# Performance work log

Hardware: AMD Instinct MI355X
Metric: run time of the kernel (lower is better)

## Reference

```python
import jax, jax.numpy as jnp
import numpy as np
from jax import lax

EPS = 1e-3  # BatchNorm1d eps from norm_fn
SPARSE_SHAPE = (41, 200, 176)  # (z, y, x)
IN_CH = 4


def _conv3d(x, w, stride, pad):
    # x: [N,C,D,H,W], w: [O,I,kd,kh,kw]
    return lax.conv_general_dilated(x, w, window_strides=stride, padding=pad,
                                    dimension_numbers=('NCDHW', 'OIDHW', 'NCDHW'))


def _bn_relu(y, bn, mask):
    # eval-mode BatchNorm1d over active voxels == per-channel affine; inactive sites
    # must stay exactly 0 in a sparse tensor, hence the final mask multiply.
    g, b, m, v = bn[0], bn[1], bn[2], bn[3]
    scale = g * lax.rsqrt(v + EPS)
    shift = b - m * scale
    y = y * scale[None, :, None, None, None] + shift[None, :, None, None, None]
    return jax.nn.relu(y) * mask


def _subm(x, mask, w, bn):
    # SubMConv3d: conv evaluated only at existing active sites; active set unchanged.
    kd, kh, kw = w.shape[2:]
    pad = [(kd // 2, kd // 2), (kh // 2, kh // 2), (kw // 2, kw // 2)]
    return _bn_relu(_conv3d(x, w, (1, 1, 1), pad), bn, mask)


def _spconv(x, mask, w, bn, stride, pad):
    # SparseConv3d: output active set = sites with >=1 active input in receptive field.
    pads = [(p, p) for p in pad]
    y = _conv3d(x, w, stride, pads)
    k = tuple(w.shape[2:])
    new_mask = lax.reduce_window(mask, 0.0, lax.max, (1, 1) + k, (1, 1) + tuple(stride),
                                 [(0, 0), (0, 0)] + pads)
    new_mask = (new_mask > 0).astype(x.dtype)
    return _bn_relu(y, bn, new_mask), new_mask


def setup_inputs() -> dict:
    key = jax.random.key(0)
    ks = jax.random.split(key, 16)
    D, H, W = SPARSE_SHAPE
    mask = (jax.random.uniform(ks[0], (1, 1, D, H, W)) < 0.02).astype(jnp.float32)
    x = jax.random.normal(ks[1], (1, IN_CH, D, H, W), jnp.float32) * mask
    specs = [(16, IN_CH, (3, 3, 3)), (16, 16, (3, 3, 3)),
             (32, 16, (3, 3, 3)), (32, 32, (3, 3, 3)), (32, 32, (3, 3, 3)),
             (64, 32, (3, 3, 3)), (64, 64, (3, 3, 3)), (64, 64, (3, 3, 3)),
             (64, 64, (3, 3, 3)), (64, 64, (3, 3, 3)), (64, 64, (3, 3, 3)),
             (128, 64, (3, 1, 1))]
    inp = {'x': x, 'mask': mask}
    for i, (co, ci, k) in enumerate(specs):
        kk = jax.random.fold_in(ks[2], i)
        fan = ci * k[0] * k[1] * k[2]
        inp['w%d' % i] = jax.random.normal(kk, (co, ci) + k, jnp.float32) / np.sqrt(fan).astype(np.float32)
        inp['bn%d' % i] = jnp.stack([
            jax.random.uniform(jax.random.fold_in(kk, 1), (co,), minval=0.5, maxval=1.5),
            jax.random.normal(jax.random.fold_in(kk, 2), (co,)) * 0.1,
            jax.random.normal(jax.random.fold_in(kk, 3), (co,)) * 0.1,
            jax.random.uniform(jax.random.fold_in(kk, 4), (co,), minval=0.5, maxval=1.5)])
    return inp


def reference(x, mask, w0, bn0, w1, bn1, w2, bn2, w3, bn3, w4, bn4, w5, bn5,
              w6, bn6, w7, bn7, w8, bn8, w9, bn9, w10, bn10, w11, bn11):
    h = _subm(x, mask, w0, bn0)                       # conv_input (subm1)
    h = _subm(h, mask, w1, bn1)                       # conv1 -> x_conv1
    h, m2 = _spconv(h, mask, w2, bn2, (2, 2, 2), (1, 1, 1))  # conv2 down
    h = _subm(h, m2, w3, bn3)
    h = _subm(h, m2, w4, bn4)                         # x_conv2
    h, m3 = _spconv(h, m2, w5, bn5, (2, 2, 2), (1, 1, 1))    # conv3 down
    h = _subm(h, m3, w6, bn6)
    h = _subm(h, m3, w7, bn7)                         # x_conv3
    h, m4 = _spconv(h, m3, w8, bn8, (2, 2, 2), (0, 1, 1))    # conv4 down
    h = _subm(h, m4, w9, bn9)
    h = _subm(h, m4, w10, bn10)                       # x_conv4
    out, _ = _spconv(h, m4, w11, bn11, (2, 1, 1), (0, 0, 0)) # conv_out
    N, C, Dd, Hh, Ww = out.shape                      # [1,128,2,25,22]
    return out.reshape(N, C * Dd, Hh, Ww)             # spatial_features [1,256,25,22]
```

## Files before the change

kernel.cpp:

```cpp
#include <hip/hip_runtime.h>

#define BS 256

constexpr int D1=41, H1=200, W1=176; constexpr int N1v=D1*H1*W1;
constexpr int D2=21, H2=100, W2=88;  constexpr int N2v=D2*H2*W2;
constexpr int D3=11, H3=50,  W3=44;  constexpr int N3v=D3*H3*W3;
constexpr int D4=5,  H4=25,  W4=22;  constexpr int N4v=D4*H4*W4;
constexpr int DOo=2, HOo=25, WOo=22;
constexpr int ROWS1=40960;

typedef __attribute__((ext_vector_type(8))) short bf16x8;
typedef __attribute__((ext_vector_type(4))) float f32x4;

__device__ __forceinline__ float bflo(unsigned int u){ return __uint_as_float(u<<16); }
__device__ __forceinline__ float bfhi(unsigned int u){ return __uint_as_float(u & 0xffff0000u); }
__device__ __forceinline__ unsigned short f2bf(float f){
  unsigned int x = __float_as_uint(f);
  x += 0x7fffu + ((x>>16)&1u);
  return (unsigned short)(x>>16);
}
__device__ __forceinline__ void acc8(float& acc, uint4 p, const float* __restrict__ wk, int stride){
  acc = fmaf(bflo(p.x), wk[0*stride], acc);
  acc = fmaf(bfhi(p.x), wk[1*stride], acc);
  acc = fmaf(bflo(p.y), wk[2*stride], acc);
  acc = fmaf(bfhi(p.y), wk[3*stride], acc);
  acc = fmaf(bflo(p.z), wk[4*stride], acc);
  acc = fmaf(bfhi(p.z), wk[5*stride], acc);
  acc = fmaf(bflo(p.w), wk[6*stride], acc);
  acc = fmaf(bfhi(p.w), wk[7*stride], acc);
}

struct PrepArgs {
  const float* w[12]; const float* bn[12];
  void* dst[12]; float* bias[12];
  int O[12], I[12], K[12], mode[12];
  int off[13];
};
__global__ void prep_all(PrepArgs a){
  int t = blockIdx.x*BS + threadIdx.x;
  if (t >= a.off[12]) return;
  int li = 0;
  while (t >= a.off[li+1]) li++;
  int e = t - a.off[li];
  int O=a.O[li], I=a.I[li], K=a.K[li], mode=a.mode[li];
  const float* w = a.w[li]; const float* bn = a.bn[li];
  if (mode == 2){
    int p = e/(O*32); int rem = e - p*(O*32); int o = rem>>5; int kk = rem&31;
    int tap = 2*p + (kk>=16 ? 1 : 0); int ci = kk&15;
    float g=bn[o], b=bn[O+o], m=bn[2*O+o], v=bn[3*O+o];
    float sc = g*rsqrtf(v+1e-3f);
    float val = (tap < 27) ? w[(o*I+ci)*K + tap]*sc : 0.f;
    ((unsigned short*)a.dst[li])[e] = f2bf(val);
    if (p==0 && kk==0) a.bias[li][o] = b - m*sc;
  } else if (mode == 3){
    int ci = e % I; int tmp = e / I; int dx = tmp % 3; tmp /= 3; int o = tmp % O; int g9 = tmp / O;
    float g=bn[o], b=bn[O+o], m=bn[2*O+o], v=bn[3*O+o];
    float sc = g*rsqrtf(v+1e-3f);
    int tap = g9*3 + dx;
    ((unsigned short*)a.dst[li])[e] = f2bf(w[(o*I+ci)*27 + tap]*sc);
    if (g9==0 && dx==0 && ci==0) a.bias[li][o] = b - m*sc;
  } else {
    int k = e % K; int rest = e / K; int ci = rest % I; int o = rest / I;
    float g=bn[o], b=bn[O+o], m=bn[2*O+o], v=bn[3*O+o];
    float sc = g*rsqrtf(v+1e-3f);
    ((float*)a.dst[li])[(k*I+ci)*O + o] = w[(o*I+ci)*K + k]*sc;
    if (ci==0 && k==0) a.bias[li][o] = b - m*sc;
  }
}

__global__ void build_list1_kernel(const float* __restrict__ mask,
                                   int* __restrict__ I1, int* __restrict__ list1,
                                   int* __restrict__ cnt){
  constexpr int PER = 16;
  __shared__ int sc[BS]; __shared__ int sbase;
  int b = blockIdx.x, t = threadIdx.x;
  int base_s = b*BS*PER;
  unsigned int bits = 0; int c = 0;
  #pragma unroll
  for (int i=0;i<PER;i++){
    int s = base_s + i*BS + t;
    bool act = (s < N1v) && (mask[s] > 0.f);
    bits |= (act?1u:0u) << i; c += act;
  }
  sc[t] = c;
  __syncthreads();
  for (int ofs=1; ofs<BS; ofs<<=1){
    int v = (t>=ofs) ? sc[t-ofs] : 0;
    __syncthreads();
    sc[t] += v;
    __syncthreads();
  }
  if (t == BS-1) sbase = atomicAdd(cnt, sc[t]);
  __syncthreads();
  int pos = sbase + sc[t] - c;
  #pragma unroll
  for (int i=0;i<PER;i++){
    if (bits & (1u<<i)){
      int s = base_s + i*BS + t;
      list1[pos] = s; I1[s] = pos+1; pos++;
    }
  }
}

template<int DI,int HI,int WI,int DOUT,int HOUT,int WOUT,int PZ,int PY,int PX>
__global__ void build_mask_kernel(const float* __restrict__ min_,
                                  float* __restrict__ mout,
                                  int* __restrict__ list, int* __restrict__ cnt1){
  constexpr int PER = 4;
  constexpr int N = DOUT*HOUT*WOUT;
  __shared__ int sc[BS]; __shared__ int sbase;
  int b = blockIdx.x, t = threadIdx.x;
  int base_s = b*BS*PER;
  unsigned int bits = 0; int c = 0;
  #pragma unroll
  for (int i=0;i<PER;i++){
    int s = base_s + i*BS + t;
    bool act = false;
    if (s < N){
      int z = s/(HOUT*WOUT); int r = s - z*(HOUT*WOUT); int y = r/WOUT; int x = r - y*WOUT;
      for (int dz=0; dz<3 && !act; dz++){ int zz = 2*z - PZ + dz; if ((unsigned)zz >= (unsigned)DI) continue;
        for (int dy=0; dy<3 && !act; dy++){ int yy = 2*y - PY + dy; if ((unsigned)yy >= (unsigned)HI) continue;
          for (int dx=0; dx<3; dx++){ int xc = 2*x - PX + dx; if ((unsigned)xc >= (unsigned)WI) continue;
            if (min_[(zz*HI+yy)*WI+xc] > 0.f){ act = true; break; }
          }}}
      mout[s] = act ? 1.f : 0.f;
    }
    bits |= (act?1u:0u) << i; c += act;
  }
  sc[t] = c;
  __syncthreads();
  for (int ofs=1; ofs<BS; ofs<<=1){
    int v = (t>=ofs) ? sc[t-ofs] : 0;
    __syncthreads();
    sc[t] += v;
    __syncthreads();
  }
  if (t == BS-1) sbase = atomicAdd(cnt1, sc[t]);
  __syncthreads();
  int pos = sbase + sc[t] - c;
  #pragma unroll
  for (int i=0;i<PER;i++){
    if (bits & (1u<<i)){
      int s = base_s + i*BS + t;
      list[pos] = s; pos++;
    }
  }
}

__global__ void subm_l0_kernel(const float* __restrict__ x,
                               const int* __restrict__ list1, const int* __restrict__ cnt,
                               const float* __restrict__ wt, const float* __restrict__ bias,
                               unsigned short* __restrict__ fout){
  int t = blockIdx.x*BS + threadIdx.x;
  int row = t >> 4, cout = t & 15;
  if (row >= cnt[0]) return;
  int s = list1[row];
  int z = s/(H1*W1); int r = s - z*(H1*W1); int y = r/W1; int xx = r - y*W1;
  float acc = bias[cout];
  for (int dz=-1; dz<=1; dz++){ int zz=z+dz; if ((unsigned)zz >= (unsigned)D1) continue;
    for (int dy=-1; dy<=1; dy++){ int yy=y+dy; if ((unsigned)yy >= (unsigned)H1) continue;
      for (int dx=-1; dx<=1; dx++){ int xc=xx+dx; if ((unsigned)xc >= (unsigned)W1) continue;
        int ns = (zz*H1+yy)*W1+xc;
        int k = ((dz+1)*3+(dy+1))*3+(dx+1);
        const float* wk = wt + k*4*16 + cout;
        #pragma unroll
        for (int ci=0; ci<4; ci++) acc = fmaf(x[ci*N1v+ns], wk[ci*16], acc);
      }}}
  fout[row*16+cout] = f2bf(fmaxf(acc, 0.f));
}

template<int COUT,int HO,int WO,int PZ,int PY,int PX,int STR,bool DENSE_OUT>
__global__ __launch_bounds__(256)
void conv_mfma_l1_kernel(const unsigned short* __restrict__ fin,
                         const int* __restrict__ I1,
                         const int* __restrict__ list, const int* __restrict__ cnt, int cidx,
                         const unsigned short* __restrict__ wbt,
                         const float* __restrict__ bias,
                         unsigned short* __restrict__ outp){
  constexpr int BP = 40;
  constexpr int NT = COUT/16;
  __shared__ __align__(16) unsigned short B[14*COUT*BP];

  int nrows = cnt[cidx];
  int row0 = blockIdx.x*64;
  if (row0 >= nrows) return;

  int t = threadIdx.x;
  int lane = t & 63, wave = t >> 6;
  int m = lane & 15, quad = lane >> 4;

  constexpr int TOT = 14*COUT*32;
  for (int e = t*8; e < TOT; e += BS*8){
    int n = e >> 5, c = e & 31;
    *(uint4*)(&B[n*BP + c]) = *(const uint4*)(wbt + e);
  }

  int row = row0 + wave*16 + m;
  bool rv = row < nrows;
  int z=0, y=0, x=0;
  {
    int s = list[rv ? row : row0];
    z = s/(HO*WO); int rem = s - z*(HO*WO); y = rem/WO; x = rem - y*WO;
  }
  __syncthreads();

  f32x4 acc[NT];
  #pragma unroll
  for (int i=0;i<NT;i++) acc[i] = (f32x4){0.f,0.f,0.f,0.f};

  #pragma unroll
  for (int p=0;p<14;p++){
    int tap = 2*p + (quad>>1);
    bf16x8 a = (bf16x8){0,0,0,0,0,0,0,0};
    if (rv && tap < 27){
      int dz = tap/9, rem = tap - dz*9, dy = rem/3, dx = rem - dy*3;
      int zz = STR*z - PZ + dz, yy = STR*y - PY + dy, xx = STR*x - PX + dx;
      if ((unsigned)zz < (unsigned)D1 && (unsigned)yy < (unsigned)H1 && (unsigned)xx < (unsigned)W1){
        int rr = I1[(zz*H1+yy)*W1+xx];
        if (rr > 0) a = *(const bf16x8*)(fin + (size_t)(rr-1)*16 + (quad&1)*8);
      }
    }
    #pragma unroll
    for (int nt=0; nt<NT; nt++){
      bf16x8 b = *(const bf16x8*)(&B[(p*COUT + nt*16 + m)*BP + quad*8]);
      acc[nt] = __builtin_amdgcn_mfma_f32_16x16x32_bf16(a, b, acc[nt], 0, 0, 0);
    }
  }

  #pragma unroll
  for (int nt=0; nt<NT; nt++){
    int cout = nt*16 + m;
    float bv = bias[cout];
    #pragma unroll
    for (int rg=0; rg<4; rg++){
      int rw = row0 + wave*16 + quad*4 + rg;
      if (rw < nrows){
        float v = fmaxf(acc[nt][rg] + bv, 0.f);
        if (DENSE_OUT){
          int s = list[rw];
          outp[(size_t)s*COUT + cout] = f2bf(v);
        } else {
          outp[(size_t)rw*COUT + cout] = f2bf(v);
        }
      }
    }
  }
}

template<int CIN,int COUT,int DI,int HI,int WI,int HO,int WO,int PZ,int PY,int PX,int STR>
__global__ __launch_bounds__(256)
void conv_mfma2_kernel(const unsigned short* __restrict__ gin,
                       const int* __restrict__ list, const int* __restrict__ cnt, int cidx,
                       const unsigned short* __restrict__ wg,
                       const float* __restrict__ bias,
                       unsigned short* __restrict__ gout){
  constexpr int KW = 3*CIN;
  constexpr int BP = KW + 8;
  constexpr int NT = COUT/16;
  constexpr int KT = KW/32;
  constexpr int PREN = (COUT*KW + BS*8 - 1)/(BS*8);
  __shared__ __align__(16) unsigned short B[2][COUT*BP];

  int nrows = cnt[cidx];
  int row0 = blockIdx.x*64;
  if (row0 >= nrows) return;

  int t = threadIdx.x;
  int lane = t & 63, wave = t >> 6;
  int m = lane & 15, quad = lane >> 4;

  #pragma unroll
  for (int i=0;i<PREN;i++){
    int e = t*8 + i*BS*8;
    if (e < COUT*KW){
      int n = e / KW, c = e - n*KW;
      *(uint4*)(&B[0][n*BP + c]) = *(const uint4*)(wg + e);
    }
  }

  int row = row0 + wave*16 + m;
  bool rv = row < nrows;
  int z=0, y=0, x=0;
  {
    int s = list[rv ? row : row0];
    z = s/(HO*WO); int rem = s - z*(HO*WO); y = rem/WO; x = rem - y*WO;
  }
  __syncthreads();

  f32x4 acc[NT];
  #pragma unroll
  for (int i=0;i<NT;i++) acc[i] = (f32x4){0.f,0.f,0.f,0.f};

  #pragma unroll
  for (int g=0; g<9; g++){
    uint4 pre[PREN];
    if (g < 8){
      const unsigned short* src = wg + (size_t)(g+1)*COUT*KW;
      #pragma unroll
      for (int i=0;i<PREN;i++){
        int e = t*8 + i*BS*8;
        pre[i] = (e < COUT*KW) ? *(const uint4*)(src + e) : (uint4){0,0,0,0};
      }
    }
    int dz = g/3, dy = g - dz*3;
    int zz = STR*z - PZ + dz, yy = STR*y - PY + dy, xx0 = STR*x - PX;
    bool zyok = rv && (unsigned)zz < (unsigned)DI && (unsigned)yy < (unsigned)HI;
    int base = ((zz*HI + yy)*WI + xx0)*CIN;
    bf16x8 av[KT];
    #pragma unroll
    for (int kt=0; kt<KT; kt++){
      constexpr int dummy = 0; (void)dummy;
      int tapx = (kt*32)/CIN;
      int kk = kt*32 + quad*8;
      av[kt] = (bf16x8){0,0,0,0,0,0,0,0};
      if (zyok && (unsigned)(xx0 + tapx) < (unsigned)WI)
        av[kt] = *(const bf16x8*)(gin + (size_t)(base + kk));
    }
    #pragma unroll
    for (int kt=0; kt<KT; kt++){
      #pragma unroll
      for (int nt=0; nt<NT; nt++){
        bf16x8 b = *(const bf16x8*)(&B[g&1][(nt*16 + m)*BP + kt*32 + quad*8]);
        acc[nt] = __builtin_amdgcn_mfma_f32_16x16x32_bf16(av[kt], b, acc[nt], 0, 0, 0);
      }
    }
    if (g < 8){
      #pragma unroll
      for (int i=0;i<PREN;i++){
        int e = t*8 + i*BS*8;
        if (e < COUT*KW){
          int n = e / KW, c = e - n*KW;
          *(uint4*)(&B[(g+1)&1][n*BP + c]) = pre[i];
        }
      }
    }
    __syncthreads();
  }

  #pragma unroll
  for (int nt=0; nt<NT; nt++){
    int cout = nt*16 + m;
    float bv = bias[cout];
    #pragma unroll
    for (int rg=0; rg<4; rg++){
      int rw = row0 + wave*16 + quad*4 + rg;
      if (rw < nrows){
        int s = list[rw];
        gout[(size_t)s*COUT + cout] = f2bf(fmaxf(acc[nt][rg] + bv, 0.f));
      }
    }
  }
}

__global__ void conv_out_kernel(const unsigned short* __restrict__ g4,
                                const float* __restrict__ m4,
                                const float* __restrict__ wt, const float* __restrict__ bias,
                                float* __restrict__ out){
  int t = blockIdx.x*BS + threadIdx.x;
  if (t >= 128*DOo*HOo*WOo) return;
  int cout = t & 127; int s = t >> 7;
  int d = s/(HOo*WOo); int r = s - d*(HOo*WOo); int h = r/WOo; int w = r - h*WOo;
  float res = 0.f;
  bool act = false;
  float acc = bias[cout];
  for (int dz=0; dz<3; dz++){
    int z4 = 2*d + dz;
    int site = (z4*H4 + h)*W4 + w;
    if (m4[site] == 0.f) continue;
    act = true;
    const uint4* fr = (const uint4*)(g4 + (size_t)site*64);
    const float* wk = wt + dz*64*128 + cout;
    #pragma unroll
    for (int q=0; q<8; q++) acc8(acc, fr[q], wk + q*8*128, 128);
  }
  if (act) res = fmaxf(acc, 0.f);
  out[((cout*DOo + d)*HOo + h)*WOo + w] = res;
}

extern "C" void kernel_launch(void* const* d_in, const int* in_sizes, int n_in,
                              void* d_out, int out_size, void* d_ws, size_t ws_size,
                              hipStream_t stream){
  const float* x    = (const float*)d_in[0];
  const float* mask = (const float*)d_in[1];
  const float* w[12]; const float* bnp[12];
  for (int i=0;i<12;i++){ w[i]=(const float*)d_in[2+2*i]; bnp[i]=(const float*)d_in[3+2*i]; }

  char* base = (char*)d_ws; size_t off = 0;
  auto alloc = [&](size_t b)->void*{ void* p = base + off; off = (off + b + 255) & ~(size_t)255; return p; };

  int* cnt   = (int*)alloc(16);
  int* I1    = (int*)alloc((size_t)N1v*4);
  unsigned short* g2a = (unsigned short*)alloc((size_t)N2v*32*2);
  unsigned short* g2b = (unsigned short*)alloc((size_t)N2v*32*2);
  unsigned short* g3a = (unsigned short*)alloc((size_t)N3v*64*2);
  unsigned short* g3b = (unsigned short*)alloc((size_t)N3v*64*2);
  unsigned short* g4a = (unsigned short*)alloc((size_t)N4v*64*2);
  unsigned short* g4b = (unsigned short*)alloc((size_t)N4v*64*2);
  size_t zero_bytes = off;
  int* list1 = (int*)alloc((size_t)ROWS1*4);
  unsigned short* f1a = (unsigned short*)alloc((size_t)ROWS1*16*2);
  unsigned short* f1b = (unsigned short*)alloc((size_t)ROWS1*16*2);
  float* m2 = (float*)alloc((size_t)N2v*4);
  int* list2 = (int*)alloc((size_t)N2v*4);
  float* m3 = (float*)alloc((size_t)N3v*4);
  int* list3 = (int*)alloc((size_t)N3v*4);
  float* m4 = (float*)alloc((size_t)N4v*4);
  int* list4 = (int*)alloc((size_t)N4v*4);

  static const int Oa[12]={16,16,32,32,32,64,64,64,64,64,64,128};
  static const int Ia[12]={ 4,16,16,32,32,32,64,64,64,64,64, 64};
  static const int Ka[12]={27,27,27,27,27,27,27,27,27,27,27,  3};
  static const int Ma[12]={ 0, 2, 2, 3, 3, 3, 3, 3, 3, 3, 3,  0};
  float* wt[12]; float* bs[12]; unsigned short* wbt[12];
  for (int i=0;i<12;i++){
    bs[i] = (float*)alloc((size_t)Oa[i]*4);
    wt[i]=nullptr; wbt[i]=nullptr;
    if (Ma[i]==0)      wt[i]  = (float*)alloc((size_t)Oa[i]*Ia[i]*Ka[i]*4);
    else if (Ma[i]==3) wbt[i] = (unsigned short*)alloc((size_t)Oa[i]*Ia[i]*27*2);
    else               wbt[i] = (unsigned short*)alloc((size_t)14*Oa[i]*32*2);
  }

  hipMemsetAsync(base, 0, zero_bytes, stream);

  PrepArgs pa;
  pa.off[0] = 0;
  for (int i=0;i<12;i++){
    pa.w[i]=w[i]; pa.bn[i]=bnp[i]; pa.bias[i]=bs[i];
    pa.O[i]=Oa[i]; pa.I[i]=Ia[i]; pa.K[i]=Ka[i]; pa.mode[i]=Ma[i];
    pa.dst[i] = (Ma[i]==0) ? (void*)wt[i] : (void*)wbt[i];
    int tot = (Ma[i]==2) ? 14*Oa[i]*32 : Oa[i]*Ia[i]*Ka[i];
    pa.off[i+1] = pa.off[i] + tot;
  }
  prep_all<<<(pa.off[12]+BS-1)/BS, BS, 0, stream>>>(pa);

  build_list1_kernel<<<(N1v + BS*16 - 1)/(BS*16), BS, 0, stream>>>(mask, I1, list1, cnt);

  subm_l0_kernel<<<(ROWS1*16)/BS, BS, 0, stream>>>(x, list1, cnt, wt[0], bs[0], f1a);
  conv_mfma_l1_kernel<16,H1,W1,1,1,1,1,false><<<ROWS1/64, 256, 0, stream>>>
      (f1a, I1, list1, cnt, 0, wbt[1], bs[1], f1b);

  build_mask_kernel<D1,H1,W1,D2,H2,W2,1,1,1><<<(N2v + BS*4 - 1)/(BS*4), BS, 0, stream>>>(mask, m2, list2, cnt+1);
  conv_mfma_l1_kernel<32,H2,W2,1,1,1,2,true><<<(N2v+63)/64, 256, 0, stream>>>
      (f1b, I1, list2, cnt, 1, wbt[2], bs[2], g2a);

  {
    int nb = (N2v + 63)/64;
    conv_mfma2_kernel<32,32,D2,H2,W2,H2,W2,1,1,1,1><<<nb, 256, 0, stream>>>(g2a, list2, cnt, 1, wbt[3], bs[3], g2b);
    conv_mfma2_kernel<32,32,D2,H2,W2,H2,W2,1,1,1,1><<<nb, 256, 0, stream>>>(g2b, list2, cnt, 1, wbt[4], bs[4], g2a);
  }

  build_mask_kernel<D2,H2,W2,D3,H3,W3,1,1,1><<<(N3v + BS*4 - 1)/(BS*4), BS, 0, stream>>>(m2, m3, list3, cnt+2);
  {
    int nb = (N3v + 63)/64;
    conv_mfma2_kernel<32,64,D2,H2,W2,H3,W3,1,1,1,2><<<nb, 256, 0, stream>>>(g2a, list3, cnt, 2, wbt[5], bs[5], g3a);
    conv_mfma2_kernel<64,64,D3,H3,W3,H3,W3,1,1,1,1><<<nb, 256, 0, stream>>>(g3a, list3, cnt, 2, wbt[6], bs[6], g3b);
    conv_mfma2_kernel<64,64,D3,H3,W3,H3,W3,1,1,1,1><<<nb, 256, 0, stream>>>(g3b, list3, cnt, 2, wbt[7], bs[7], g3a);
  }

  build_mask_kernel<D3,H3,W3,D4,H4,W4,0,1,1><<<(N4v + BS*4 - 1)/(BS*4), BS, 0, stream>>>(m3, m4, list4, cnt+3);
  {
    int nb = (N4v + 63)/64;
    conv_mfma2_kernel<64,64,D3,H3,W3,H4,W4,0,1,1,2><<<nb, 256, 0, stream>>>(g3a, list4, cnt, 3, wbt[8], bs[8], g4a);
    conv_mfma2_kernel<64,64,D4,H4,W4,H4,W4,1,1,1,1><<<nb, 256, 0, stream>>>(g4a, list4, cnt, 3, wbt[9], bs[9], g4b);
    conv_mfma2_kernel<64,64,D4,H4,W4,H4,W4,1,1,1,1><<<nb, 256, 0, stream>>>(g4b, list4, cnt, 3, wbt[10], bs[10], g4a);
  }

  conv_out_kernel<<<(128*DOo*HOo*WOo)/BS, BS, 0, stream>>>(g4a, m4, wt[11], bs[11], (float*)d_out);
}
```

Baseline: 438.9 us.

## Build downsampled masks by scattering from active lists; restructure layer-0 conv per voxel

Output masks for the strided sparse convs are now built by having each active input voxel scatter 1s to the output sites it touches, followed by a separate compaction kernel, instead of every output site gathering over a 27-voxel window of the dense input mask. The mask buffers are moved into the memset region so they start at zero. The first submanifold conv now computes all 16 output channels per thread with weights staged in shared memory, so each input voxel is read once instead of 16 times. This adds an extra kernel launch per downsampling stage and register pressure from the 16-wide accumulator.

```diff
diff --git a/kernel.cpp b/kernel.cpp
--- a/kernel.cpp
+++ b/kernel.cpp
@@ -103,30 +103,30 @@
 }
 
 template<int DI,int HI,int WI,int DOUT,int HOUT,int WOUT,int PZ,int PY,int PX>
-__global__ void build_mask_kernel(const float* __restrict__ min_,
-                                  float* __restrict__ mout,
-                                  int* __restrict__ list, int* __restrict__ cnt1){
-  constexpr int PER = 4;
-  constexpr int N = DOUT*HOUT*WOUT;
+__global__ void scatter_mask_kernel(const int* __restrict__ list, const int* __restrict__ cnt, int cidx,
+                                    float* __restrict__ mout){
+  int t = blockIdx.x*BS + threadIdx.x;
+  if (t >= cnt[cidx]) return;
+  int s = list[t];
+  int zz = s/(HI*WI); int rem = s - zz*(HI*WI); int yy = rem/WI; int xx = rem - yy*WI;
+  int az = zz + PZ, ay = yy + PY, ax = xx + PX;
+  int zlo = (az-2) <= 0 ? 0 : (az-1)/2;  int zhi = min(DOUT-1, az/2);
+  int ylo = (ay-2) <= 0 ? 0 : (ay-1)/2;  int yhi = min(HOUT-1, ay/2);
+  int xlo = (ax-2) <= 0 ? 0 : (ax-1)/2;  int xhi = min(WOUT-1, ax/2);
+  for (int zo=zlo; zo<=zhi; zo++)
+    for (int yo=ylo; yo<=yhi; yo++)
+      for (int xo=xlo; xo<=xhi; xo++)
+        mout[(zo*HOUT+yo)*WOUT+xo] = 1.f;
+}
+
+template<int N>
+__global__ void compact_mask_kernel(const float* __restrict__ mout,
+                                    int* __restrict__ list, int* __restrict__ cnt1){
   __shared__ int sc[BS]; __shared__ int sbase;
   int b = blockIdx.x, t = threadIdx.x;
-  int base_s = b*BS*PER;
-  unsigned int bits = 0; int c = 0;
-  #pragma unroll
-  for (int i=0;i<PER;i++){
-    int s = base_s + i*BS + t;
-    bool act = false;
-    if (s < N){
-      int z = s/(HOUT*WOUT); int r = s - z*(HOUT*WOUT); int y = r/WOUT; int x = r - y*WOUT;
-      for (int dz=0; dz<3 && !act; dz++){ int zz = 2*z - PZ + dz; if ((unsigned)zz >= (unsigned)DI) continue;
-        for (int dy=0; dy<3 && !act; dy++){ int yy = 2*y - PY + dy; if ((unsigned)yy >= (unsigned)HI) continue;
-          for (int dx=0; dx<3; dx++){ int xc = 2*x - PX + dx; if ((unsigned)xc >= (unsigned)WI) continue;
-            if (min_[(zz*HI+yy)*WI+xc] > 0.f){ act = true; break; }
-          }}}
-      mout[s] = act ? 1.f : 0.f;
-    }
-    bits |= (act?1u:0u) << i; c += act;
-  }
+  int s = b*BS + t;
+  bool act = (s < N) && (mout[s] > 0.f);
+  int c = act ? 1 : 0;
   sc[t] = c;
   __syncthreads();
   for (int ofs=1; ofs<BS; ofs<<=1){
@@ -137,36 +137,39 @@
   }
   if (t == BS-1) sbase = atomicAdd(cnt1, sc[t]);
   __syncthreads();
-  int pos = sbase + sc[t] - c;
-  #pragma unroll
-  for (int i=0;i<PER;i++){
-    if (bits & (1u<<i)){
-      int s = base_s + i*BS + t;
-      list[pos] = s; pos++;
-    }
-  }
+  if (act) list[sbase + sc[t] - 1] = s;
 }
 
 __global__ void subm_l0_kernel(const float* __restrict__ x,
                                const int* __restrict__ list1, const int* __restrict__ cnt,
                                const float* __restrict__ wt, const float* __restrict__ bias,
                                unsigned short* __restrict__ fout){
-  int t = blockIdx.x*BS + threadIdx.x;
-  int row = t >> 4, cout = t & 15;
+  __shared__ float Wl[27*4*16];
+  __shared__ float Bl[16];
+  int t = threadIdx.x;
+  for (int e=t; e<27*4*16; e+=BS) Wl[e] = wt[e];
+  if (t < 16) Bl[t] = bias[t];
+  __syncthreads();
+  int row = blockIdx.x*BS + t;
   if (row >= cnt[0]) return;
   int s = list1[row];
   int z = s/(H1*W1); int r = s - z*(H1*W1); int y = r/W1; int xx = r - y*W1;
-  float acc = bias[cout];
+  float acc[16];
+  #pragma unroll
+  for (int o=0;o<16;o++) acc[o] = Bl[o];
   for (int dz=-1; dz<=1; dz++){ int zz=z+dz; if ((unsigned)zz >= (unsigned)D1) continue;
     for (int dy=-1; dy<=1; dy++){ int yy=y+dy; if ((unsigned)yy >= (unsigned)H1) continue;
       for (int dx=-1; dx<=1; dx++){ int xc=xx+dx; if ((unsigned)xc >= (unsigned)W1) continue;
         int ns = (zz*H1+yy)*W1+xc;
         int k = ((dz+1)*3+(dy+1))*3+(dx+1);
-        const float* wk = wt + k*4*16 + cout;
+        float x0 = x[ns], x1 = x[N1v+ns], x2 = x[2*N1v+ns], x3 = x[3*N1v+ns];
+        const float* wk = Wl + k*64;
         #pragma unroll
-        for (int ci=0; ci<4; ci++) acc = fmaf(x[ci*N1v+ns], wk[ci*16], acc);
+        for (int o=0;o<16;o++)
+          acc[o] = fmaf(x0, wk[o], fmaf(x1, wk[16+o], fmaf(x2, wk[32+o], fmaf(x3, wk[48+o], acc[o]))));
       }}}
-  fout[row*16+cout] = f2bf(fmaxf(acc, 0.f));
+  #pragma unroll
+  for (int o=0;o<16;o++) fout[row*16+o] = f2bf(fmaxf(acc[o], 0.f));
 }
 
 template<int COUT,int HO,int WO,int PZ,int PY,int PX,int STR,bool DENSE_OUT>
@@ -309,7 +312,6 @@
     bf16x8 av[KT];
     #pragma unroll
     for (int kt=0; kt<KT; kt++){
-      constexpr int dummy = 0; (void)dummy;
       int tapx = (kt*32)/CIN;
       int kk = kt*32 + quad*8;
       av[kt] = (bf16x8){0,0,0,0,0,0,0,0};
@@ -396,15 +398,15 @@
   unsigned short* g3b = (unsigned short*)alloc((size_t)N3v*64*2);
   unsigned short* g4a = (unsigned short*)alloc((size_t)N4v*64*2);
   unsigned short* g4b = (unsigned short*)alloc((size_t)N4v*64*2);
+  float* m2 = (float*)alloc((size_t)N2v*4);
+  float* m3 = (float*)alloc((size_t)N3v*4);
+  float* m4 = (float*)alloc((size_t)N4v*4);
   size_t zero_bytes = off;
   int* list1 = (int*)alloc((size_t)ROWS1*4);
   unsigned short* f1a = (unsigned short*)alloc((size_t)ROWS1*16*2);
   unsigned short* f1b = (unsigned short*)alloc((size_t)ROWS1*16*2);
-  float* m2 = (float*)alloc((size_t)N2v*4);
   int* list2 = (int*)alloc((size_t)N2v*4);
-  float* m3 = (float*)alloc((size_t)N3v*4);
   int* list3 = (int*)alloc((size_t)N3v*4);
-  float* m4 = (float*)alloc((size_t)N4v*4);
   int* list4 = (int*)alloc((size_t)N4v*4);
 
   static const int Oa[12]={16,16,32,32,32,64,64,64,64,64,64,128};
@@ -435,11 +437,12 @@
 
   build_list1_kernel<<<(N1v + BS*16 - 1)/(BS*16), BS, 0, stream>>>(mask, I1, list1, cnt);
 
-  subm_l0_kernel<<<(ROWS1*16)/BS, BS, 0, stream>>>(x, list1, cnt, wt[0], bs[0], f1a);
+  subm_l0_kernel<<<(ROWS1+BS-1)/BS, BS, 0, stream>>>(x, list1, cnt, wt[0], bs[0], f1a);
   conv_mfma_l1_kernel<16,H1,W1,1,1,1,1,false><<<ROWS1/64, 256, 0, stream>>>
       (f1a, I1, list1, cnt, 0, wbt[1], bs[1], f1b);
 
-  build_mask_kernel<D1,H1,W1,D2,H2,W2,1,1,1><<<(N2v + BS*4 - 1)/(BS*4), BS, 0, stream>>>(mask, m2, list2, cnt+1);
+  scatter_mask_kernel<D1,H1,W1,D2,H2,W2,1,1,1><<<(ROWS1+BS-1)/BS, BS, 0, stream>>>(list1, cnt, 0, m2);
+  compact_mask_kernel<N2v><<<(N2v+BS-1)/BS, BS, 0, stream>>>(m2, list2, cnt+1);
   conv_mfma_l1_kernel<32,H2,W2,1,1,1,2,true><<<(N2v+63)/64, 256, 0, stream>>>
       (f1b, I1, list2, cnt, 1, wbt[2], bs[2], g2a);
 
@@ -449,7 +452,8 @@
     conv_mfma2_kernel<32,32,D2,H2,W2,H2,W2,1,1,1,1><<<nb, 256, 0, stream>>>(g2b, list2, cnt, 1, wbt[4], bs[4], g2a);
   }
 
-  build_mask_kernel<D2,H2,W2,D3,H3,W3,1,1,1><<<(N3v + BS*4 - 1)/(BS*4), BS, 0, stream>>>(m2, m3, list3, cnt+2);
+  scatter_mask_kernel<D2,H2,W2,D3,H3,W3,1,1,1><<<(N2v+BS-1)/BS, BS, 0, stream>>>(list2, cnt, 1, m3);
+  compact_mask_kernel<N3v><<<(N3v+BS-1)/BS, BS, 0, stream>>>(m3, list3, cnt+2);
   {
     int nb = (N3v + 63)/64;
     conv_mfma2_kernel<32,64,D2,H2,W2,H3,W3,1,1,1,2><<<nb, 256, 0, stream>>>(g2a, list3, cnt, 2, wbt[5], bs[5], g3a);
@@ -457,7 +461,8 @@
     conv_mfma2_kernel<64,64,D3,H3,W3,H3,W3,1,1,1,1><<<nb, 256, 0, stream>>>(g3b, list3, cnt, 2, wbt[7], bs[7], g3a);
   }
 
-  build_mask_kernel<D3,H3,W3,D4,H4,W4,0,1,1><<<(N4v + BS*4 - 1)/(BS*4), BS, 0, stream>>>(m3, m4, list4, cnt+3);
+  scatter_mask_kernel<D3,H3,W3,D4,H4,W4,0,1,1><<<(N3v+BS-1)/BS, BS, 0, stream>>>(list3, cnt, 2, m4);
+  compact_mask_kernel<N4v><<<(N4v+BS-1)/BS, BS, 0, stream>>>(m4, list4, cnt+3);
   {
     int nb = (N4v + 63)/64;
     conv_mfma2_kernel<64,64,D3,H3,W3,H4,W4,0,1,1,2><<<nb, 256, 0, stream>>>(g3a, list4, cnt, 3, wbt[8], bs[8], g4a);
```

After: 440.0 us. No clear change (+0.3%).
